# Optimization experiments

Measured on AMD Instinct MI355X. Metric: run time of the kernel, lower is better.

## Reference

```python
import jax, jax.numpy as jnp
import numpy as np

N = 50000      # nodes
E = 1200000    # edges
G = 256        # graphs in batch
H = 64         # hidden_dim
F_IN = 5       # input_dim
L = 3          # num deep GCN layers
EPS_BN = 1e-5
EPS_MSG = 1e-7

def setup_inputs() -> dict:
    key = jax.random.key(0)
    ks = jax.random.split(key, 12)
    r = lambda i, shp, s=0.1: jax.random.normal(ks[i], shp, jnp.float32) * s
    return {
        "x": jax.random.normal(ks[0], (N, F_IN), jnp.float32),
        "edge_index": jax.random.randint(ks[1], (2, E), 0, N),
        "batch_idx": jnp.sort(jax.random.randint(ks[2], (N,), 0, G)),
        "conv1_W": r(3, (F_IN, H)), "conv1_b": jnp.zeros((H,), jnp.float32),
        "bn1_g": jnp.ones((H,), jnp.float32), "bn1_b": jnp.zeros((H,), jnp.float32),
        "ln_g": jnp.ones((L, H), jnp.float32), "ln_b": jnp.zeros((L, H), jnp.float32),
        "prelu_a": jnp.full((L, H), 0.25, jnp.float32),
        "gen_t": jnp.ones((L,), jnp.float32),
        "mlp_W1": r(4, (L, H, 2 * H)), "mlp_b1": jnp.zeros((L, 2 * H), jnp.float32),
        "mlp_bn_g": jnp.ones((L, 2 * H), jnp.float32), "mlp_bn_b": jnp.zeros((L, 2 * H), jnp.float32),
        "mlp_W2": r(5, (L, 2 * H, H)), "mlp_b2": jnp.zeros((L, H), jnp.float32),
        "lin1_W": r(6, ((L + 1) * H * 2, 2 * H)), "lin1_b": jnp.zeros((2 * H,), jnp.float32),
        "lin2_W": r(7, (2 * H, H)), "lin2_b": jnp.zeros((H,), jnp.float32),
        "out_W": r(8, (H, 1)), "out_b": jnp.zeros((1,), jnp.float32),
    }

def _layernorm(x, g, b):
    mu = jnp.mean(x, axis=-1, keepdims=True)
    var = jnp.mean(jnp.square(x - mu), axis=-1, keepdims=True)
    return (x - mu) * jax.lax.rsqrt(var + EPS_BN) * g + b

def _prelu(x, a):
    return jnp.where(x >= 0, x, a * x)

def _bn_eval(x, g, b):
    # eval-mode BatchNorm with running_mean=0, running_var=1
    return x * (g / jnp.sqrt(1.0 + EPS_BN)) + b

def reference(x, edge_index, batch_idx, conv1_W, conv1_b, bn1_g, bn1_b,
              ln_g, ln_b, prelu_a, gen_t, mlp_W1, mlp_b1, mlp_bn_g, mlp_bn_b,
              mlp_W2, mlp_b2, lin1_W, lin1_b, lin2_W, lin2_b, out_W, out_b):
    n = x.shape[0]
    src, dst = edge_index[0], edge_index[1]

    # ---- GCNConv (with self loops, symmetric normalization) ----
    loops = jnp.arange(n)
    row = jnp.concatenate([src, loops])  # [E+N]
    col = jnp.concatenate([dst, loops])
    h = x @ conv1_W
    deg = jax.ops.segment_sum(jnp.ones_like(col, jnp.float32), col, num_segments=n)
    dinv = jnp.where(deg > 0, deg ** -0.5, 0.0)
    norm = dinv[row] * dinv[col]
    h = jax.ops.segment_sum(h[row] * norm[:, None], col, num_segments=n) + conv1_b
    h = _bn_eval(h, bn1_g, bn1_b)
    h = jax.nn.relu(h)

    xs = [h]
    # ---- DeepGCNLayer (res+) x L, GENConv with softmax aggregation ----
    for i in range(ln_g.shape[0]):
        u = _layernorm(h, ln_g[i], ln_b[i])
        u = _prelu(u, prelu_a[i])
        msg = jax.nn.relu(u[src]) + EPS_MSG            # [E, H]
        sc = msg * gen_t[i]
        m = jax.ops.segment_max(sc, dst, num_segments=n)
        e = jnp.exp(sc - m[dst])
        s = jax.ops.segment_sum(e, dst, num_segments=n)
        alpha = e / s[dst]                             # segment-wise softmax per channel
        agg = jax.ops.segment_sum(msg * alpha, dst, num_segments=n) + u  # root add
        z = agg @ mlp_W1[i] + mlp_b1[i]
        z = _bn_eval(z, mlp_bn_g[i], mlp_bn_b[i])
        z = jax.nn.relu(z)
        z = z @ mlp_W2[i] + mlp_b2[i]
        h = h + z                                      # res+
        xs.append(h)

    # ---- JumpingKnowledge cat + global mean/max pool ----
    xc = jnp.concatenate(xs, axis=1)                   # [N, 4H]
    cnt = jax.ops.segment_sum(jnp.ones((n,), jnp.float32), batch_idx, num_segments=G)
    xmean = jax.ops.segment_sum(xc, batch_idx, num_segments=G) / jnp.maximum(cnt, 1.0)[:, None]
    xmax = jax.ops.segment_max(xc, batch_idx, num_segments=G)
    xmax = jnp.where(jnp.isfinite(xmax), xmax, 0.0)
    p = jnp.concatenate([xmean, xmax], axis=1)         # [G, 8H]

    # ---- readout MLP (dropout off in eval) ----
    p = jax.nn.relu(p @ lin1_W + lin1_b)
    p = jax.nn.relu(p @ lin2_W + lin2_b)
    return p @ out_W + out_b
```

## Files before the change

kernel.cpp:

```cpp
#include <hip/hip_runtime.h>
#include <math.h>

#define NND 50000
#define NE  1200000
#define NG  256
#define H   64
#define H2  128
#define H4  256
#define H8  512
#define FIN 5
#define EPS_BN 1e-5f
#define EPS_MSG 1e-7f
#define NB 196
#define NXP 8
#define DPART 6250
#define EC1 4688
#define EC4 1172
#define ELLC 72
#define PC 8
#define MT 64

typedef _Float16 half8 __attribute__((ext_vector_type(8)));
typedef _Float16 half4 __attribute__((ext_vector_type(4)));
typedef float floatx4 __attribute__((ext_vector_type(4)));
typedef unsigned uintx4 __attribute__((ext_vector_type(4)));


__global__ void k_setup(const int* __restrict__ batch, const int* __restrict__ ei,
                        int* next, unsigned* __restrict__ epk, int* __restrict__ gstart,
                        const float* __restrict__ x, float* __restrict__ xp,
                        const float* __restrict__ W1, const float* __restrict__ W2,
                        _Float16* __restrict__ w1f, _Float16* __restrict__ w2f) {
    int b = blockIdx.x, t = threadIdx.x;
    if (b < NB) {
        int n = b * 256 + t;
        if (n < NND) {
            next[n] = 0;
            float a0 = x[n * FIN + 0], a1 = x[n * FIN + 1], a2 = x[n * FIN + 2];
            float a3 = x[n * FIN + 3], a4 = x[n * FIN + 4];
            *(float4*)&xp[n * 8] = make_float4(a0, a1, a2, a3);
            *(float4*)&xp[n * 8 + 4] = make_float4(a4, 0.f, 0.f, 0.f);
        }
        return;
    }
    if (b == NB || b == NB + 1) {
        int g = (b - NB) * 256 + t;
        if (g > NG) return;
        int lo = 0, hi = NND;
        while (lo < hi) { int mid = (lo + hi) >> 1; if (batch[mid] < g) lo = mid + 1; else hi = mid; }
        gstart[g] = lo;
        return;
    }
    if (b < NB + 2 + 12) {
        int tt = (b - NB - 2) * 256 + t;
        if (tt >= 3 * 16 * 64) return;
        int lane = tt & 63, fr = (tt >> 6) & 15, l = tt >> 10;
        {
            int jt = fr >> 1, kf = fr & 1;
            int j = jt * 16 + (lane & 15);
            int k0 = kf * 32 + (lane >> 4) * 8;
#pragma unroll
            for (int i = 0; i < 8; i++)
                w1f[(((size_t)l * 16 + jt * 2 + kf) * 64 + lane) * 8 + i] =
                    (_Float16)W1[(size_t)l * H * H2 + (k0 + i) * H2 + j];
        }
        {
            int ct = fr >> 2, k2f = fr & 3;
            int c = ct * 16 + (lane & 15);
            int k0 = k2f * 32 + (lane >> 4) * 8;
#pragma unroll
            for (int i = 0; i < 8; i++)
                w2f[(((size_t)l * 16 + ct * 4 + k2f) * 64 + lane) * 8 + i] =
                    (_Float16)W2[(size_t)l * H2 * H + (k0 + i) * H + c];
        }
        return;
    }
    int e = (b - NB - 14) * 256 + t;
    if (e < NE) {
        unsigned s = (unsigned)ei[e];
        unsigned d = (unsigned)ei[NE + e];
        epk[e] = (s << 16) | d;
    }
}


__global__ void k_scatter_p(const unsigned* __restrict__ epk, int* next,
                            unsigned short* __restrict__ ell) {
    int b = blockIdx.x;
    int g = b & (NXP - 1);
    int base = (((b >> 3) * 256) + threadIdx.x) << 2;
    if (base >= NE) return;
    uintx4 v4 = __builtin_nontemporal_load((const uintx4*)(epk + base));
#pragma unroll
    for (int k = 0; k < 4; k++) {
        unsigned v = v4[k];
        int d = (int)(v & 0xFFFFu);
        if ((unsigned)(d - g * DPART) < (unsigned)DPART) {
            int slot = atomicAdd(&next[d], 1);
            if (slot < ELLC) ell[(size_t)d * ELLC + slot] = (unsigned short)(v >> 16);
        }
    }
}

__global__ void k_dinv(const int* __restrict__ next, float* __restrict__ dinv) {
    int n = blockIdx.x * 256 + threadIdx.x;
    if (n >= NND) return;
    dinv[n] = rsqrtf((float)next[n] + 1.0f);
}


__global__ void k_gcn(const int* __restrict__ deg, const unsigned short* __restrict__ ell,
                      const float* __restrict__ xp, const float* __restrict__ dinv,
                      const float* __restrict__ W,
                      const float* __restrict__ cb, const float* __restrict__ bg,
                      const float* __restrict__ bb,
                      const float* __restrict__ lg, const float* __restrict__ lb,
                      const float* __restrict__ pa,
                      float* __restrict__ xc, float* __restrict__ u,
                      _Float16* __restrict__ u_h) {
    int d = (blockIdx.x * blockDim.x + threadIdx.x) >> 6;
    int lane = threadIdx.x & 63;
    if (d >= NND) return;
    int dg = min(deg[d], ELLC);
    size_t base = (size_t)d * ELLC;
    float xw0 = 0.f, xw1 = 0.f, xw2 = 0.f, xw3 = 0.f, xw4 = 0.f;
    for (int i = lane; i < dg; i += 64) {
        int s = (int)ell[base + i];
        float dv = dinv[s];
        float4 a = *(const float4*)&xp[s * 8];
        float a4 = xp[s * 8 + 4];
        xw0 += a.x * dv; xw1 += a.y * dv; xw2 += a.z * dv;
        xw3 += a.w * dv; xw4 += a4 * dv;
    }
#pragma unroll
    for (int off = 1; off <= 32; off <<= 1) {
        xw0 += __shfl_xor(xw0, off, 64);
        xw1 += __shfl_xor(xw1, off, 64);
        xw2 += __shfl_xor(xw2, off, 64);
        xw3 += __shfl_xor(xw3, off, 64);
        xw4 += __shfl_xor(xw4, off, 64);
    }
    float dd = dinv[d];
    float4 xa = *(const float4*)&xp[d * 8];
    float xa4 = xp[d * 8 + 4];
    xw0 += dd * xa.x; xw1 += dd * xa.y; xw2 += dd * xa.z;
    xw3 += dd * xa.w; xw4 += dd * xa4;
    float s_ = xw0 * W[0 * H + lane] + xw1 * W[1 * H + lane] + xw2 * W[2 * H + lane]
             + xw3 * W[3 * H + lane] + xw4 * W[4 * H + lane];
    float v = s_ * dd + cb[lane];
    v = v * (bg[lane] * rsqrtf(1.f + EPS_BN)) + bb[lane];
    float x0 = fmaxf(v, 0.f);
    xc[(size_t)d * H4 + lane] = x0;
    float sum = x0, sq = x0 * x0;
#pragma unroll
    for (int off = 32; off >= 1; off >>= 1) {
        sum += __shfl_xor(sum, off, 64);
        sq  += __shfl_xor(sq,  off, 64);
    }
    float mu  = sum * (1.f / H);
    float var = sq * (1.f / H) - mu * mu;
    float rs = rsqrtf(var + EPS_BN);
    float y = (x0 - mu) * rs * lg[lane] + lb[lane];
    y = (y >= 0.f) ? y : pa[lane] * y;
    u[d * H + lane] = y;
    u_h[(size_t)d * H + lane] = (_Float16)y;
}


__global__ void k_gen(const int* __restrict__ deg, const unsigned short* __restrict__ ell,
                      const float* __restrict__ u, const _Float16* __restrict__ u_h,
                      const float* __restrict__ tptr, int li, float* __restrict__ ua) {
    int d = (blockIdx.x * blockDim.x + threadIdx.x) >> 6;
    int lane = threadIdx.x & 63;
    if (d >= NND) return;
    int q = lane & 15, eg = lane >> 4;
    float t = tptr[li];
    int dg = min(deg[d], ELLC);
    size_t base = (size_t)d * ELLC;
    float4 s4 = {0.f, 0.f, 0.f, 0.f}, n4 = {0.f, 0.f, 0.f, 0.f};
    for (int i0 = 0; i0 < dg; i0 += 64) {
        int idx = i0 + lane;
        int csrv = (idx < dg) ? (int)ell[base + idx] : 0;
        int chunk = min(64, dg - i0);
        for (int j = 0; j < chunk; j += 16) {
            half4 uv[4]; bool ok[4];
#pragma unroll
            for (int bb2 = 0; bb2 < 4; bb2++) {
                int e_rel = j + 4 * bb2 + eg;
                int s = __shfl(csrv, e_rel, 64);
                ok[bb2] = (e_rel < chunk);
                uv[bb2] = (half4){0, 0, 0, 0};
                if (ok[bb2]) uv[bb2] = *(const half4*)&u_h[(size_t)s * H + 4 * q];
            }
#pragma unroll
            for (int bb2 = 0; bb2 < 4; bb2++) {
                if (ok[bb2]) {
                    float m0 = fmaxf((float)uv[bb2][0], 0.f) + EPS_MSG;
                    float m1 = fmaxf((float)uv[bb2][1], 0.f) + EPS_MSG;
                    float m2 = fmaxf((float)uv[bb2][2], 0.f) + EPS_MSG;
                    float m3 = fmaxf((float)uv[bb2][3], 0.f) + EPS_MSG;
                    float e0 = __expf(m0 * t - 8.f);
                    float e1 = __expf(m1 * t - 8.f);
                    float e2 = __expf(m2 * t - 8.f);
                    float e3 = __expf(m3 * t - 8.f);
                    s4.x += e0; s4.y += e1; s4.z += e2; s4.w += e3;
                    n4.x += m0 * e0; n4.y += m1 * e1; n4.z += m2 * e2; n4.w += m3 * e3;
                }
            }
        }
    }
#pragma unroll
    for (int off = 16; off <= 32; off <<= 1) {
        s4.x += __shfl_xor(s4.x, off, 64); s4.y += __shfl_xor(s4.y, off, 64);
        s4.z += __shfl_xor(s4.z, off, 64); s4.w += __shfl_xor(s4.w, off, 64);
        n4.x += __shfl_xor(n4.x, off, 64); n4.y += __shfl_xor(n4.y, off, 64);
        n4.z += __shfl_xor(n4.z, off, 64); n4.w += __shfl_xor(n4.w, off, 64);
    }
    if (eg == 0) {
        float4 us = *(const float4*)&u[d * H + 4 * q];
        float4 o;
        o.x = us.x + ((s4.x > 0.f) ? n4.x / s4.x : 0.f);
        o.y = us.y + ((s4.y > 0.f) ? n4.y / s4.y : 0.f);
        o.z = us.z + ((s4.z > 0.f) ? n4.z / s4.z : 0.f);
        o.w = us.w + ((s4.w > 0.f) ? n4.w / s4.w : 0.f);
        *(float4*)&ua[d * H + 4 * q] = o;
    }
}


__global__ void __launch_bounds__(256)
k_mlp(const float* __restrict__ ua,
      const _Float16* __restrict__ w1f, const _Float16* __restrict__ w2f,
      const float* __restrict__ b1,
      const float* __restrict__ bng, const float* __restrict__ bnb,
      const float* __restrict__ b2,
      float* __restrict__ xc, int slice,
      const float* __restrict__ lg, const float* __restrict__ lb,
      const float* __restrict__ pa, float* __restrict__ u_next,
      _Float16* __restrict__ u_h, int do_ln) {
    __shared__ _Float16 a1[4][2][64][8];
    __shared__ _Float16 a2[4][4][64][8];
    int t = threadIdx.x;
    int w = t >> 6, l = t & 63;
    int nb = blockIdx.x * MT;
    int c_in = l & 15, quad = l >> 4;
    bool wvalid = (nb + 16 * w) < NND;

    {
        int n = t >> 2;
        int k0 = (t & 3) * 16;
        int gn = nb + n;
        float4 v0 = {0,0,0,0}, v1 = v0, v2 = v0, v3 = v0;
        if (gn < NND) {
            v0 = *(const float4*)&ua[gn * H + k0];
            v1 = *(const float4*)&ua[gn * H + k0 + 4];
            v2 = *(const float4*)&ua[gn * H + k0 + 8];
            v3 = *(const float4*)&ua[gn * H + k0 + 12];
        }
        int mt = n >> 4, kf = k0 >> 5, g0 = (k0 >> 3) & 3;
        half8 h0 = {(_Float16)v0.x, (_Float16)v0.y, (_Float16)v0.z, (_Float16)v0.w,
                    (_Float16)v1.x, (_Float16)v1.y, (_Float16)v1.z, (_Float16)v1.w};
        half8 h1 = {(_Float16)v2.x, (_Float16)v2.y, (_Float16)v2.z, (_Float16)v2.w,
                    (_Float16)v3.x, (_Float16)v3.y, (_Float16)v3.z, (_Float16)v3.w};
        *(half8*)&a1[mt][kf][(n & 15) + 16 * g0][0] = h0;
        *(half8*)&a1[mt][kf][(n & 15) + 16 * (g0 + 1)][0] = h1;
    }

    floatx4 acc[8];
#pragma unroll
    for (int jt = 0; jt < 8; jt++) acc[jt] = (floatx4){0.f, 0.f, 0.f, 0.f};
    half8 af0 = *(half8*)&a1[w][0][l][0];
    half8 af1 = *(half8*)&a1[w][1][l][0];
#pragma unroll
    for (int jt = 0; jt < 8; jt++) {
        half8 bf0 = *(const half8*)&w1f[((size_t)(jt * 2 + 0) * 64 + l) * 8];
        half8 bf1 = *(const half8*)&w1f[((size_t)(jt * 2 + 1) * 64 + l) * 8];
        acc[jt] = __builtin_amdgcn_mfma_f32_16x16x32_f16(af0, bf0, acc[jt], 0, 0, 0);
        acc[jt] = __builtin_amdgcn_mfma_f32_16x16x32_f16(af1, bf1, acc[jt], 0, 0, 0);
    }

    {
        float bns = rsqrtf(1.f + EPS_BN);
#pragma unroll
        for (int jt = 0; jt < 8; jt++) {
            int j = jt * 16 + c_in;
            float b1v = b1[j], bsv = bng[j] * bns, bbv = bnb[j];
            int kf2 = jt >> 1;
            int lp = 16 * ((2 * jt + (c_in >> 3)) & 3);
            int ii = c_in & 7;
#pragma unroll
            for (int reg = 0; reg < 4; reg++) {
                float z = fmaxf((acc[jt][reg] + b1v) * bsv + bbv, 0.f);
                a2[w][kf2][quad * 4 + reg + lp][ii] = (_Float16)z;
            }
        }
    }

    floatx4 acc2[4];
#pragma unroll
    for (int ct = 0; ct < 4; ct++) acc2[ct] = (floatx4){0.f, 0.f, 0.f, 0.f};
    half8 a2f[4];
#pragma unroll
    for (int k2f = 0; k2f < 4; k2f++) a2f[k2f] = *(half8*)&a2[w][k2f][l][0];
#pragma unroll
    for (int ct = 0; ct < 4; ct++) {
#pragma unroll
        for (int k2f = 0; k2f < 4; k2f++) {
            half8 bfr = *(const half8*)&w2f[((size_t)(ct * 4 + k2f) * 64 + l) * 8];
            acc2[ct] = __builtin_amdgcn_mfma_f32_16x16x32_f16(a2f[k2f], bfr, acc2[ct], 0, 0, 0);
        }
    }

    float vv[4][4];
#pragma unroll
    for (int ct = 0; ct < 4; ct++) {
        int c = ct * 16 + c_in;
        float b2v = b2[c];
#pragma unroll
        for (int reg = 0; reg < 4; reg++) {
            int node = nb + 16 * w + quad * 4 + reg;
            float v = 0.f;
            if (wvalid) {
                v = xc[(size_t)node * H4 + slice * H + c] + acc2[ct][reg] + b2v;
                xc[(size_t)node * H4 + (slice + 1) * H + c] = v;
            }
            vv[ct][reg] = v;
        }
    }
    if (do_ln) {
#pragma unroll
        for (int reg = 0; reg < 4; reg++) {
            float s = (vv[0][reg] + vv[1][reg]) + (vv[2][reg] + vv[3][reg]);
            float q = (vv[0][reg] * vv[0][reg] + vv[1][reg] * vv[1][reg]) +
                      (vv[2][reg] * vv[2][reg] + vv[3][reg] * vv[3][reg]);
#pragma unroll
            for (int off = 1; off <= 8; off <<= 1) {
                s += __shfl_xor(s, off, 64);
                q += __shfl_xor(q, off, 64);
            }
            float mu = s * (1.f / H);
            float var = q * (1.f / H) - mu * mu;
            float rs = rsqrtf(var + EPS_BN);
            int node = nb + 16 * w + quad * 4 + reg;
#pragma unroll
            for (int ct = 0; ct < 4; ct++) {
                int c = ct * 16 + c_in;
                float y = (vv[ct][reg] - mu) * rs * lg[c] + lb[c];
                y = (y >= 0.f) ? y : pa[c] * y;
                if (wvalid) {
                    u_next[node * H + c] = y;
                    u_h[(size_t)node * H + c] = (_Float16)y;
                }
            }
        }
    }
}


__global__ void __launch_bounds__(256)
k_pool1(const float* __restrict__ xc, const int* __restrict__ gstart,
        float* __restrict__ psum_p, float* __restrict__ pmax_p) {
    __shared__ float4 ssum[256];
    __shared__ float4 smax[256];
    int b = blockIdx.x;
    int g = b >> 3, k = b & (PC - 1);
    int t = threadIdx.x;
    int start = gstart[g], end = gstart[g + 1];
    int len = end - start;
    int c0 = start + (len * k) / PC;
    int c1 = start + (len * (k + 1)) / PC;
    int q = t & 63, sub = t >> 6;
    float4 sum = {0.f, 0.f, 0.f, 0.f};
    float4 mx = {-INFINITY, -INFINITY, -INFINITY, -INFINITY};
    for (int n = c0 + sub; n < c1; n += 4) {
        float4 v = *(const float4*)&xc[(size_t)n * H4 + 4 * q];
        sum.x += v.x; sum.y += v.y; sum.z += v.z; sum.w += v.w;
        mx.x = fmaxf(mx.x, v.x); mx.y = fmaxf(mx.y, v.y);
        mx.z = fmaxf(mx.z, v.z); mx.w = fmaxf(mx.w, v.w);
    }
    ssum[t] = sum; smax[t] = mx;
    __syncthreads();
    if (t < 64) {
        float4 s0 = ssum[t], s1 = ssum[t + 64], s2 = ssum[t + 128], s3 = ssum[t + 192];
        float4 m0 = smax[t], m1 = smax[t + 64], m2 = smax[t + 128], m3 = smax[t + 192];
        float4 S, M;
        S.x = (s0.x + s1.x) + (s2.x + s3.x);
        S.y = (s0.y + s1.y) + (s2.y + s3.y);
        S.z = (s0.z + s1.z) + (s2.z + s3.z);
        S.w = (s0.w + s1.w) + (s2.w + s3.w);
        M.x = fmaxf(fmaxf(m0.x, m1.x), fmaxf(m2.x, m3.x));
        M.y = fmaxf(fmaxf(m0.y, m1.y), fmaxf(m2.y, m3.y));
        M.z = fmaxf(fmaxf(m0.z, m1.z), fmaxf(m2.z, m3.z));
        M.w = fmaxf(fmaxf(m0.w, m1.w), fmaxf(m2.w, m3.w));
        *(float4*)&psum_p[(size_t)b * H4 + 4 * q] = S;
        *(float4*)&pmax_p[(size_t)b * H4 + 4 * q] = M;
    }
}

__global__ void __launch_bounds__(256)
k_readout(const float* __restrict__ psum_p, const float* __restrict__ pmax_p,
          const int* __restrict__ gstart,
          const float* __restrict__ W1, const float* __restrict__ b1,
          const float* __restrict__ W2, const float* __restrict__ b2,
          const float* __restrict__ Wo, const float* __restrict__ bo,
          float* __restrict__ out) {
    __shared__ float p0_l[H8];
    __shared__ float p1part[2][H2];
    __shared__ float p1_l[H2];
    __shared__ float p2part[4][H];
    __shared__ float p2_l[H];
    int g = blockIdx.x;
    int t = threadIdx.x;

    {
        float s = 0.f, m = -INFINITY;
#pragma unroll
        for (int k = 0; k < PC; k++) {
            s += psum_p[(size_t)(g * PC + k) * H4 + t];
            m = fmaxf(m, pmax_p[(size_t)(g * PC + k) * H4 + t]);
        }
        int cnt = gstart[g + 1] - gstart[g];
        p0_l[t] = s / fmaxf((float)cnt, 1.f);
        p0_l[H4 + t] = (cnt > 0) ? m : 0.f;
    }
    __syncthreads();

    {
        int j = t & 127, h = t >> 7;
        float acc = 0.f;
        int k0 = h * 256;
        for (int k = 0; k < 256; k++) acc += p0_l[k0 + k] * W1[(k0 + k) * H2 + j];
        p1part[h][j] = acc;
    }
    __syncthreads();
    if (t < H2) p1_l[t] = fmaxf(p1part[0][t] + p1part[1][t] + b1[t], 0.f);
    __syncthreads();

    {
        int c = t & 63, h = t >> 6;
        float acc = 0.f;
        int k0 = h * 32;
        for (int k = 0; k < 32; k++) acc += p1_l[k0 + k] * W2[(k0 + k) * H + c];
        p2part[h][c] = acc;
    }
    __syncthreads();
    if (t < H) p2_l[t] = fmaxf(((p2part[0][t] + p2part[1][t]) + (p2part[2][t] + p2part[3][t])) + b2[t], 0.f);
    __syncthreads();

    if (t < 64) {
        float v = p2_l[t] * Wo[t];
#pragma unroll
        for (int off = 32; off >= 1; off >>= 1) v += __shfl_xor(v, off, 64);
        if (t == 0) out[g] = v + bo[0];
    }
}

extern "C" void kernel_launch(void* const* d_in, const int* in_sizes, int n_in,
                              void* d_out, int out_size, void* d_ws, size_t ws_size,
                              hipStream_t stream) {
    const float* x       = (const float*)d_in[0];
    const int*   ei      = (const int*)d_in[1];
    const int*   batch   = (const int*)d_in[2];
    const float* conv1_W = (const float*)d_in[3];
    const float* conv1_b = (const float*)d_in[4];
    const float* bn1_g   = (const float*)d_in[5];
    const float* bn1_b   = (const float*)d_in[6];
    const float* ln_g    = (const float*)d_in[7];
    const float* ln_b    = (const float*)d_in[8];
    const float* prelu_a = (const float*)d_in[9];
    const float* gen_t   = (const float*)d_in[10];
    const float* mlp_W1  = (const float*)d_in[11];
    const float* mlp_b1  = (const float*)d_in[12];
    const float* mlp_bng = (const float*)d_in[13];
    const float* mlp_bnb = (const float*)d_in[14];
    const float* mlp_W2  = (const float*)d_in[15];
    const float* mlp_b2  = (const float*)d_in[16];
    const float* lin1_W  = (const float*)d_in[17];
    const float* lin1_b  = (const float*)d_in[18];
    const float* lin2_W  = (const float*)d_in[19];
    const float* lin2_b  = (const float*)d_in[20];
    const float* out_W   = (const float*)d_in[21];
    const float* out_b   = (const float*)d_in[22];
    float* out = (float*)d_out;

    float* ws   = (float*)d_ws;
    float* xc   = ws;
    float* u    = xc + (size_t)NND * H4;
    float* ua   = u + (size_t)NND * H;
    float* xp   = ua + (size_t)NND * H;
    float* dinv = xp + (size_t)NND * 8;
    int* next   = (int*)(dinv + NND);
    int* gstart = next + NND;
    unsigned* epk = (unsigned*)(gstart + NG + 1);
    unsigned short* ell = (unsigned short*)(epk + NE);
    uintptr_t wb = (uintptr_t)(ell + (size_t)NND * ELLC);
    wb = (wb + 15) & ~(uintptr_t)15;
    _Float16* w1f = (_Float16*)wb;
    _Float16* w2f = w1f + 3 * 8192;
    _Float16* u_h = w2f + 3 * 8192;
    uintptr_t pb = (uintptr_t)(u_h + (size_t)NND * H);
    pb = (pb + 15) & ~(uintptr_t)15;
    float* psum_p = (float*)pb;
    float* pmax_p = psum_p + (size_t)NG * PC * H4;

    const int B = 256;
    const int gN   = (NND + B - 1) / B;
    const int gNH  = (NND * H) / B;
    const int gMLP = (NND + MT - 1) / MT;
    const int gEP4 = NXP * EC4;

    k_setup<<<NB + 2 + 12 + EC1, B, 0, stream>>>(batch, ei, next, epk, gstart,
                                                 x, xp, mlp_W1, mlp_W2, w1f, w2f);
    k_scatter_p<<<gEP4, B, 0, stream>>>(epk, next, ell);
    k_dinv<<<gN, B, 0, stream>>>(next, dinv);

    k_gcn<<<gNH, B, 0, stream>>>(next, ell, xp, dinv, conv1_W, conv1_b, bn1_g, bn1_b,
                                 ln_g, ln_b, prelu_a, xc, u, u_h);

    for (int i = 0; i < 3; i++) {
        k_gen<<<gNH, B, 0, stream>>>(next, ell, u, u_h, gen_t, i, ua);
        int do_ln = (i < 2) ? 1 : 0;
        k_mlp<<<gMLP, B, 0, stream>>>(ua,
                                      w1f + (size_t)i * 8192, w2f + (size_t)i * 8192,
                                      mlp_b1 + i * H2,
                                      mlp_bng + i * H2, mlp_bnb + i * H2,
                                      mlp_b2 + i * H,
                                      xc, i,
                                      ln_g + (i + 1) * H, ln_b + (i + 1) * H,
                                      prelu_a + (i + 1) * H, u, u_h, do_ln);
    }

    k_pool1<<<NG * PC, B, 0, stream>>>(xc, gstart, psum_p, pmax_p);
    k_readout<<<NG, B, 0, stream>>>(psum_p, pmax_p, gstart,
                                    lin1_W, lin1_b, lin2_W, lin2_b, out_W, out_b, out);
}
```

Measured before the change: 377.4 us.

## Build ELL adjacency via two-pass tile binning with shared-memory assembly

Replaces the packed-edge pass, the partitioned global-atomic scatter and the separate dinv kernel with a two-stage binning scheme. Edges are first bucketed into 256-node destination tiles using shared-memory counters and one global atomic per tile per block. Each tile's ELL rows are then assembled in LDS and written out coalesced, with deg and dinv computed in the same kernel. This removes per-edge global atomics and the scattered 2-byte stores, but adds a fixed per-tile capacity (TCAP) that could silently drop edges if a tile overflows.

After: 347.6 us. -7.9%, faster.

```diff
diff --git a/kernel.cpp b/kernel.cpp
--- a/kernel.cpp
+++ b/kernel.cpp
@@ -12,10 +12,10 @@
 #define EPS_BN 1e-5f
 #define EPS_MSG 1e-7f
 #define NB 196
-#define NXP 8
-#define DPART 6250
-#define EC1 4688
-#define EC4 1172
+#define TILES 196
+#define TCAP 7168
+#define EPB 4096
+#define NB1 293
 #define ELLC 72
 #define PC 8
 #define MT 64
@@ -23,11 +23,9 @@
 typedef _Float16 half8 __attribute__((ext_vector_type(8)));
 typedef _Float16 half4 __attribute__((ext_vector_type(4)));
 typedef float floatx4 __attribute__((ext_vector_type(4)));
-typedef unsigned uintx4 __attribute__((ext_vector_type(4)));
-
-
-__global__ void k_setup(const int* __restrict__ batch, const int* __restrict__ ei,
-                        int* next, unsigned* __restrict__ epk, int* __restrict__ gstart,
+
+
+__global__ void k_setup(const int* __restrict__ batch, int* tilecur, int* __restrict__ gstart,
                         const float* __restrict__ x, float* __restrict__ xp,
                         const float* __restrict__ W1, const float* __restrict__ W2,
                         _Float16* __restrict__ w1f, _Float16* __restrict__ w2f) {
@@ -35,7 +33,6 @@
     if (b < NB) {
         int n = b * 256 + t;
         if (n < NND) {
-            next[n] = 0;
             float a0 = x[n * FIN + 0], a1 = x[n * FIN + 1], a2 = x[n * FIN + 2];
             float a3 = x[n * FIN + 3], a4 = x[n * FIN + 4];
             *(float4*)&xp[n * 8] = make_float4(a0, a1, a2, a3);
@@ -44,6 +41,7 @@
         return;
     }
     if (b == NB || b == NB + 1) {
+        if (b == NB && t < TILES) tilecur[t] = 0;
         int g = (b - NB) * 256 + t;
         if (g > NG) return;
         int lo = 0, hi = NND;
@@ -51,61 +49,87 @@
         gstart[g] = lo;
         return;
     }
-    if (b < NB + 2 + 12) {
-        int tt = (b - NB - 2) * 256 + t;
-        if (tt >= 3 * 16 * 64) return;
-        int lane = tt & 63, fr = (tt >> 6) & 15, l = tt >> 10;
-        {
-            int jt = fr >> 1, kf = fr & 1;
-            int j = jt * 16 + (lane & 15);
-            int k0 = kf * 32 + (lane >> 4) * 8;
-#pragma unroll
-            for (int i = 0; i < 8; i++)
-                w1f[(((size_t)l * 16 + jt * 2 + kf) * 64 + lane) * 8 + i] =
-                    (_Float16)W1[(size_t)l * H * H2 + (k0 + i) * H2 + j];
-        }
-        {
-            int ct = fr >> 2, k2f = fr & 3;
-            int c = ct * 16 + (lane & 15);
-            int k0 = k2f * 32 + (lane >> 4) * 8;
-#pragma unroll
-            for (int i = 0; i < 8; i++)
-                w2f[(((size_t)l * 16 + ct * 4 + k2f) * 64 + lane) * 8 + i] =
-                    (_Float16)W2[(size_t)l * H2 * H + (k0 + i) * H + c];
-        }
-        return;
-    }
-    int e = (b - NB - 14) * 256 + t;
-    if (e < NE) {
-        unsigned s = (unsigned)ei[e];
-        unsigned d = (unsigned)ei[NE + e];
-        epk[e] = (s << 16) | d;
-    }
-}
-
-
-__global__ void k_scatter_p(const unsigned* __restrict__ epk, int* next,
-                            unsigned short* __restrict__ ell) {
-    int b = blockIdx.x;
-    int g = b & (NXP - 1);
-    int base = (((b >> 3) * 256) + threadIdx.x) << 2;
-    if (base >= NE) return;
-    uintx4 v4 = __builtin_nontemporal_load((const uintx4*)(epk + base));
-#pragma unroll
-    for (int k = 0; k < 4; k++) {
-        unsigned v = v4[k];
-        int d = (int)(v & 0xFFFFu);
-        if ((unsigned)(d - g * DPART) < (unsigned)DPART) {
-            int slot = atomicAdd(&next[d], 1);
-            if (slot < ELLC) ell[(size_t)d * ELLC + slot] = (unsigned short)(v >> 16);
-        }
-    }
-}
-
-__global__ void k_dinv(const int* __restrict__ next, float* __restrict__ dinv) {
-    int n = blockIdx.x * 256 + threadIdx.x;
-    if (n >= NND) return;
-    dinv[n] = rsqrtf((float)next[n] + 1.0f);
+    int tt = (b - NB - 2) * 256 + t;
+    if (tt >= 3 * 16 * 64) return;
+    int lane = tt & 63, fr = (tt >> 6) & 15, l = tt >> 10;
+    {
+        int jt = fr >> 1, kf = fr & 1;
+        int j = jt * 16 + (lane & 15);
+        int k0 = kf * 32 + (lane >> 4) * 8;
+#pragma unroll
+        for (int i = 0; i < 8; i++)
+            w1f[(((size_t)l * 16 + jt * 2 + kf) * 64 + lane) * 8 + i] =
+                (_Float16)W1[(size_t)l * H * H2 + (k0 + i) * H2 + j];
+    }
+    {
+        int ct = fr >> 2, k2f = fr & 3;
+        int c = ct * 16 + (lane & 15);
+        int k0 = k2f * 32 + (lane >> 4) * 8;
+#pragma unroll
+        for (int i = 0; i < 8; i++)
+            w2f[(((size_t)l * 16 + ct * 4 + k2f) * 64 + lane) * 8 + i] =
+                (_Float16)W2[(size_t)l * H2 * H + (k0 + i) * H + c];
+    }
+}
+
+
+__global__ void __launch_bounds__(256)
+k_bin1(const int* __restrict__ ei, int* tilecur, unsigned* __restrict__ tilebuf) {
+    __shared__ int cnt[TILES];
+    __shared__ int base[TILES];
+    int b = blockIdx.x, t = threadIdx.x;
+    for (int i = t; i < TILES; i += 256) cnt[i] = 0;
+    __syncthreads();
+    int e0 = b * EPB;
+#pragma unroll
+    for (int r = 0; r < EPB / 256; r++) {
+        int e = e0 + r * 256 + t;
+        if (e < NE) atomicAdd(&cnt[ei[NE + e] >> 8], 1);
+    }
+    __syncthreads();
+    for (int i = t; i < TILES; i += 256) {
+        base[i] = atomicAdd(&tilecur[i], cnt[i]);
+        cnt[i] = 0;
+    }
+    __syncthreads();
+#pragma unroll
+    for (int r = 0; r < EPB / 256; r++) {
+        int e = e0 + r * 256 + t;
+        if (e < NE) {
+            int s = ei[e], d = ei[NE + e];
+            int tile = d >> 8;
+            int pos = base[tile] + atomicAdd(&cnt[tile], 1);
+            if (pos < TCAP)
+                tilebuf[(size_t)tile * TCAP + pos] = ((unsigned)s << 8) | (unsigned)(d & 255);
+        }
+    }
+}
+
+__global__ void __launch_bounds__(256)
+k_bin2(const int* __restrict__ tilecur, const unsigned* __restrict__ tilebuf,
+       unsigned short* __restrict__ ell, int* __restrict__ deg, float* __restrict__ dinv) {
+    __shared__ unsigned short ell_l[256 * ELLC];
+    __shared__ int cnt[256];
+    int tile = blockIdx.x, t = threadIdx.x;
+    cnt[t] = 0;
+    __syncthreads();
+    int n = min(tilecur[tile], TCAP);
+    for (int i = t; i < n; i += 256) {
+        unsigned v = tilebuf[(size_t)tile * TCAP + i];
+        int dl = v & 255u;
+        int slot = atomicAdd(&cnt[dl], 1);
+        if (slot < ELLC) ell_l[dl * ELLC + slot] = (unsigned short)(v >> 8);
+    }
+    __syncthreads();
+    const unsigned* s32 = (const unsigned*)ell_l;
+    unsigned* d32 = (unsigned*)(ell + (size_t)tile * 256 * ELLC);
+    for (int i = t; i < 256 * ELLC / 2; i += 256) d32[i] = s32[i];
+    int d = tile * 256 + t;
+    if (d < NND) {
+        int c = min(cnt[t], ELLC);
+        deg[d] = c;
+        dinv[d] = rsqrtf((float)cnt[t] + 1.0f);
+    }
 }
 
 
@@ -121,7 +145,7 @@
     int d = (blockIdx.x * blockDim.x + threadIdx.x) >> 6;
     int lane = threadIdx.x & 63;
     if (d >= NND) return;
-    int dg = min(deg[d], ELLC);
+    int dg = deg[d];
     size_t base = (size_t)d * ELLC;
     float xw0 = 0.f, xw1 = 0.f, xw2 = 0.f, xw3 = 0.f, xw4 = 0.f;
     for (int i = lane; i < dg; i += 64) {
@@ -175,7 +199,7 @@
     if (d >= NND) return;
     int q = lane & 15, eg = lane >> 4;
     float t = tptr[li];
-    int dg = min(deg[d], ELLC);
+    int dg = deg[d];
     size_t base = (size_t)d * ELLC;
     float4 s4 = {0.f, 0.f, 0.f, 0.f}, n4 = {0.f, 0.f, 0.f, 0.f};
     for (int i0 = 0; i0 < dg; i0 += 64) {
@@ -489,11 +513,12 @@
     float* ua   = u + (size_t)NND * H;
     float* xp   = ua + (size_t)NND * H;
     float* dinv = xp + (size_t)NND * 8;
-    int* next   = (int*)(dinv + NND);
-    int* gstart = next + NND;
-    unsigned* epk = (unsigned*)(gstart + NG + 1);
-    unsigned short* ell = (unsigned short*)(epk + NE);
-    uintptr_t wb = (uintptr_t)(ell + (size_t)NND * ELLC);
+    int* deg    = (int*)(dinv + NND);
+    int* gstart = deg + NND;
+    int* tilecur = gstart + NG + 1;
+    unsigned* tilebuf = (unsigned*)(tilecur + TILES);
+    unsigned short* ell = (unsigned short*)(tilebuf + (size_t)TILES * TCAP);
+    uintptr_t wb = (uintptr_t)(ell + (size_t)TILES * 256 * ELLC);
     wb = (wb + 15) & ~(uintptr_t)15;
     _Float16* w1f = (_Float16*)wb;
     _Float16* w2f = w1f + 3 * 8192;
@@ -504,21 +529,19 @@
     float* pmax_p = psum_p + (size_t)NG * PC * H4;
 
     const int B = 256;
-    const int gN   = (NND + B - 1) / B;
     const int gNH  = (NND * H) / B;
     const int gMLP = (NND + MT - 1) / MT;
-    const int gEP4 = NXP * EC4;
-
-    k_setup<<<NB + 2 + 12 + EC1, B, 0, stream>>>(batch, ei, next, epk, gstart,
-                                                 x, xp, mlp_W1, mlp_W2, w1f, w2f);
-    k_scatter_p<<<gEP4, B, 0, stream>>>(epk, next, ell);
-    k_dinv<<<gN, B, 0, stream>>>(next, dinv);
-
-    k_gcn<<<gNH, B, 0, stream>>>(next, ell, xp, dinv, conv1_W, conv1_b, bn1_g, bn1_b,
+
+    k_setup<<<NB + 2 + 12, B, 0, stream>>>(batch, tilecur, gstart, x, xp,
+                                           mlp_W1, mlp_W2, w1f, w2f);
+    k_bin1<<<NB1, B, 0, stream>>>(ei, tilecur, tilebuf);
+    k_bin2<<<TILES, B, 0, stream>>>(tilecur, tilebuf, ell, deg, dinv);
+
+    k_gcn<<<gNH, B, 0, stream>>>(deg, ell, xp, dinv, conv1_W, conv1_b, bn1_g, bn1_b,
                                  ln_g, ln_b, prelu_a, xc, u, u_h);
 
     for (int i = 0; i < 3; i++) {
-        k_gen<<<gNH, B, 0, stream>>>(next, ell, u, u_h, gen_t, i, ua);
+        k_gen<<<gNH, B, 0, stream>>>(deg, ell, u, u_h, gen_t, i, ua);
         int do_ln = (i < 2) ? 1 : 0;
         k_mlp<<<gMLP, B, 0, stream>>>(ua,
                                       w1f + (size_t)i * 8192, w2f + (size_t)i * 8192,
```
